# Performance work log

Measured on AMD Instinct MI355X. Metric: run time of the kernel, lower is better.

The kernel has to match this reference:

```python
import jax, jax.numpy as jnp
import numpy as np

N = 32768      # total atoms in batch
D_IN = 1024    # input feature dimension
H1 = 512       # encoder/decoder hidden width
LAT = 128      # latent dimension
D_OUT = 1024   # output dimension
E = 4          # number of unique element symbols (experts)


def _xavier(key, shape):
    # torch.nn.init.xavier_uniform_ on Linear weights
    fan_in, fan_out = shape[-2], shape[-1]
    limit = np.sqrt(6.0 / (fan_in + fan_out)).astype(np.float32)
    return jax.random.uniform(key, shape, jnp.float32, -limit, limit)


def setup_inputs() -> dict:
    key = jax.random.key(0)
    ks = jax.random.split(key, 8)
    X = jax.random.normal(ks[0], (N, D_IN), jnp.float32)
    sym_ids = jax.random.randint(ks[1], (N,), 0, E)
    # stacked per-symbol (expert) weights: topology 1024->512->128->512->1024
    We1 = _xavier(ks[2], (E, D_IN, H1));  be1 = jnp.zeros((E, H1), jnp.float32)
    We2 = _xavier(ks[3], (E, H1, LAT));   be2 = jnp.zeros((E, LAT), jnp.float32)
    Wd1 = _xavier(ks[4], (E, LAT, H1));   bd1 = jnp.zeros((E, H1), jnp.float32)
    Wd2 = _xavier(ks[5], (E, H1, D_OUT)); bd2 = jnp.zeros((E, D_OUT), jnp.float32)
    return {"X": X, "sym_ids": sym_ids,
            "We1": We1, "be1": be1, "We2": We2, "be2": be2,
            "Wd1": Wd1, "bd1": bd1, "Wd2": Wd2, "bd2": bd2}


def reference(X, sym_ids, We1, be1, We2, be2, Wd1, bd1, Wd2, bd2):
    # Dense MoE-style dispatch: compute every expert on the full batch (E is
    # tiny and fixed), then select each atom's own-symbol output. Same math as
    # the per-atom Python-loop routing in the original forward.
    def expert(e):
        h = jax.nn.relu(X @ We1[e] + be1[e])          # [N, H1]  encoder layer 1
        z = jax.nn.relu(h @ We2[e] + be2[e])          # [N, LAT] latent (encoder layer 2)
        d = jax.nn.relu(z @ Wd1[e] + bd1[e])          # [N, H1]  decoder layer 1
        return d @ Wd2[e] + bd2[e]                    # [N, D_OUT] final Linear, no activation

    outs = jnp.stack([expert(e) for e in range(E)])   # [E, N, D_OUT]
    # route: pick expert sym_ids[n] for atom n
    return jnp.take_along_axis(outs, sym_ids[None, :, None], axis=0)[0]
```

## Files before the change

### kernel.cpp

```cpp
#include <hip/hip_runtime.h>
#include <hip/hip_bf16.h>
#include <stdint.h>

typedef __bf16 bf16x8 __attribute__((ext_vector_type(8)));
typedef float  f32x4  __attribute__((ext_vector_type(4)));

#define NATOMS  32768
#define NEXP    4
#define MAXROWS (NATOMS + NEXP*256)
#define MB256   (MAXROWS/256)
#define MB128   (MAXROWS/128)
#define MGRP    ((MB256 + 7)/8)
#define PXBLK   (MAXROWS/2)

#define WS_HDR   0u
#define WS_PERM  1024u
#define WS_W1T   136192u
#define WS_W2T   (WS_W1T + 4194304u)
#define WS_W3T   (WS_W2T + 524288u)
#define WS_W4T   (WS_W3T + 524288u)
#define WS_H     (WS_W4T + 4194304u)
#define WS_D     WS_H
#define WS_XB    (WS_H + 34603008u)

__device__ __forceinline__ unsigned short f2bf(float f){
  union { float f; uint32_t u; } v; v.f = f;
  uint32_t r = v.u + 0x7fffu + ((v.u >> 16) & 1u);
  return (unsigned short)(r >> 16);
}
__device__ __forceinline__ uint32_t pk2(float a, float b){
  return (uint32_t)f2bf(a) | ((uint32_t)f2bf(b) << 16);
}
__device__ __forceinline__ void glds16(const void* g, void* l){
  __builtin_amdgcn_global_load_lds(
      (const __attribute__((address_space(1))) uint32_t*)g,
      (__attribute__((address_space(3))) uint32_t*)l, 16, 0, 0);
}

__global__ __launch_bounds__(1024) void route_kernel(const int* __restrict__ sym,
                                                     int* __restrict__ hdr,
                                                     int* __restrict__ perm){
  __shared__ unsigned wsumA[16], wsumB[16];
  __shared__ unsigned wexclA[16], wexclB[16];
  __shared__ int pof[NEXP+1];
  __shared__ int tot[NEXP];
  const int t = threadIdx.x;
  const int lane = t & 63, w = t >> 6;
  int c0=0,c1=0,c2=0,c3=0;
  const int base = t*32;
  for (int i=0;i<32;++i){
    int s = sym[base+i];
    c0 += (s==0); c1 += (s==1); c2 += (s==2); c3 += (s==3);
  }
  unsigned pA = (unsigned)c0 | ((unsigned)c1<<16);
  unsigned pB = (unsigned)c2 | ((unsigned)c3<<16);
  unsigned iA = pA, iB = pB;
  #pragma unroll
  for (int d=1; d<64; d<<=1){
    unsigned uA = __shfl_up(iA, d, 64);
    unsigned uB = __shfl_up(iB, d, 64);
    if (lane >= d){ iA += uA; iB += uB; }
  }
  unsigned exA = iA - pA, exB = iB - pB;
  if (lane == 63){ wsumA[w] = iA; wsumB[w] = iB; }
  __syncthreads();
  if (w == 0 && lane < 16){
    unsigned vA = wsumA[lane], vB = wsumB[lane];
    unsigned jA = vA, jB = vB;
    #pragma unroll
    for (int d=1; d<16; d<<=1){
      unsigned uA = __shfl_up(jA, d, 64);
      unsigned uB = __shfl_up(jB, d, 64);
      if (lane >= d){ jA += uA; jB += uB; }
    }
    wexclA[lane] = jA - vA; wexclB[lane] = jB - vB;
    if (lane == 15){
      tot[0] = (int)(jA & 0xFFFFu); tot[1] = (int)(jA >> 16);
      tot[2] = (int)(jB & 0xFFFFu); tot[3] = (int)(jB >> 16);
      int o = 0; pof[0] = 0;
      for (int e=0;e<NEXP;++e){ o += (tot[e]+255)&~255; pof[e+1]=o; }
      for (int e=0;e<=NEXP;++e) hdr[e]=pof[e];
    }
  }
  __syncthreads();
  const unsigned bA = wexclA[w] + exA, bB = wexclB[w] + exB;
  int p0 = pof[0] + (int)(bA & 0xFFFFu);
  int p1 = pof[1] + (int)(bA >> 16);
  int p2 = pof[2] + (int)(bB & 0xFFFFu);
  int p3 = pof[3] + (int)(bB >> 16);
  for (int i=t; i<MAXROWS; i+=1024) perm[i] = -1;
  __syncthreads();
  for (int i=0;i<32;++i){
    int a = base+i; int s = sym[a];
    if      (s==0) perm[p0++] = a;
    else if (s==1) perm[p1++] = a;
    else if (s==2) perm[p2++] = a;
    else           perm[p3++] = a;
  }
}

template<int K, int NO>
__device__ __forceinline__ void wtile(const float* __restrict__ W,
                                      unsigned short* __restrict__ Bt,
                                      int b, unsigned short (*tile)[65]){
  const int nx = NO/64, ny = K/64;
  const int e = b / (nx*ny), rem = b % (nx*ny);
  const int k0 = (rem / nx) * 64;
  const int n0 = (rem % nx) * 64;
  const int t  = threadIdx.x;
  const int c  = t & 63;
  const float* Wb = W + ((size_t)e*K + k0)*NO + n0;
  #pragma unroll
  for (int i=0;i<16;++i){
    int r = (t>>6) + i*4;
    tile[r][c] = f2bf(Wb[(size_t)r*NO + c]);
  }
  __syncthreads();
  unsigned short* Bb = Bt + ((size_t)e*NO + n0)*K + k0;
  #pragma unroll
  for (int i=0;i<16;++i){
    int r = (t>>6) + i*4;
    Bb[(size_t)r*K + c] = tile[c][r];
  }
}

__global__ __launch_bounds__(256) void setup_convert(
    const float* __restrict__ X,   unsigned short* __restrict__ Xb,
    const float* __restrict__ We1, unsigned short* __restrict__ W1t,
    const float* __restrict__ We2, unsigned short* __restrict__ W2t,
    const float* __restrict__ Wd1, unsigned short* __restrict__ W3t,
    const float* __restrict__ Wd2, unsigned short* __restrict__ W4t,
    const int* __restrict__ perm)
{
  __shared__ unsigned short tile[64][65];
  int b = blockIdx.x;
  const int t = threadIdx.x;
  if (b < PXBLK){
    const int row = b*2 + (t >> 7);
    const int c8  = (t & 127) * 8;
    const int a   = perm[row];
    uint4 o;
    if (a >= 0){
      const float* src = X + (size_t)a*1024 + c8;
      float4 f0 = *(const float4*)src, f1 = *(const float4*)(src + 4);
      o.x = pk2(f0.x,f0.y); o.y = pk2(f0.z,f0.w);
      o.z = pk2(f1.x,f1.y); o.w = pk2(f1.z,f1.w);
    } else {
      o = make_uint4(0u,0u,0u,0u);
    }
    *(uint4*)&Xb[(size_t)row*1024 + c8] = o;
    return;
  }
  b -= PXBLK;
  if (b < 512){ wtile<1024, 512>(We1, W1t, b, tile); return; }
  b -= 512;
  if (b <  64){ wtile< 512, 128>(We2, W2t, b, tile); return; }
  b -= 64;
  if (b <  64){ wtile< 128, 512>(Wd1, W3t, b, tile); return; }
  b -= 64;
  wtile< 512,1024>(Wd2, W4t, b, tile);
}

template<int K, int NO, int NT, bool RELU, bool FINAL>
__global__ __launch_bounds__(512, 4) void gemm_big(
    const unsigned short* __restrict__ A,
    const unsigned short* __restrict__ Bt,
    const float* __restrict__ bias,
    unsigned short* __restrict__ Cb,
    float* __restrict__ Cf,
    const int* __restrict__ hdr,
    const int* __restrict__ perm)
{
  __shared__ __align__(16) unsigned short smem[256*64 + 128*64];
  __shared__ int sperm[256];
  unsigned short* As = smem;
  unsigned short* Bs = smem + 256*64;

  const int b = blockIdx.x;
  const int grp = b / (8*NT), rem = b % (8*NT);
  const int rowblk = grp*8 + (rem & 7);
  const int row0 = rowblk * 256;
  if (row0 >= hdr[NEXP]) return;
  const int ntile = rem >> 3;
  const int e = (row0 >= hdr[1]) + (row0 >= hdr[2]) + (row0 >= hdr[3]);
  const int n0 = ntile * 128;

  const int t = threadIdx.x;
  const int lane = t & 63, wid = t >> 6;

  if constexpr (FINAL){
    if (t < 256) sperm[t] = perm[row0 + t];
    __syncthreads();
  }

  const int l8 = lane >> 3;
  const int scoff = (((lane & 7) ^ l8) << 3);

  const unsigned short* asrc[4];
  #pragma unroll
  for (int i=0;i<4;++i)
    asrc[i] = A + (size_t)(row0 + wid*32 + i*8 + l8)*K + scoff;
  const unsigned short* bsrc[2];
  #pragma unroll
  for (int i=0;i<2;++i)
    bsrc[i] = Bt + ((size_t)e*NO + n0 + wid*16 + i*8 + l8)*K + scoff;

  const int lr   = lane & 15;
  const int sgrp = lane >> 4;
  const int wr   = (wid >> 1) * 64;
  const int wc   = (wid & 1) * 64;

  f32x4 acc[4][4];
  const f32x4 z4 = {0.f,0.f,0.f,0.f};
  #pragma unroll
  for (int mi=0;mi<4;++mi)
    #pragma unroll
    for (int ni=0;ni<4;++ni) acc[mi][ni] = z4;

  #pragma unroll 1
  for (int kt = 0; kt < K/64; ++kt){
    __syncthreads();
    #pragma unroll
    for (int i=0;i<4;++i)
      glds16(asrc[i] + kt*64, As + (wid*4+i)*512);
    #pragma unroll
    for (int i=0;i<2;++i)
      glds16(bsrc[i] + kt*64, Bs + (wid*2+i)*512);
    __syncthreads();

    #pragma unroll
    for (int kk=0;kk<2;++kk){
      bf16x8 af[4], bfr[4];
      const int s = kk*4 + sgrp;
      #pragma unroll
      for (int mi=0;mi<4;++mi){
        int R = wr + mi*16 + lr;
        af[mi] = *(const bf16x8*)&As[R*64 + ((s ^ (R & 7)) << 3)];
      }
      #pragma unroll
      for (int ni=0;ni<4;++ni){
        int Cc = wc + ni*16 + lr;
        bfr[ni] = *(const bf16x8*)&Bs[Cc*64 + ((s ^ (Cc & 7)) << 3)];
      }
      #pragma unroll
      for (int mi=0;mi<4;++mi)
        #pragma unroll
        for (int ni=0;ni<4;++ni)
          acc[mi][ni] = __builtin_amdgcn_mfma_f32_16x16x32_bf16(af[mi], bfr[ni], acc[mi][ni], 0, 0, 0);
    }
  }

  __syncthreads();
  if constexpr (FINAL){
    float* stf = (float*)smem;
    #pragma unroll
    for (int qr=0; qr<4; ++qr){
      if ((wid >> 1) == qr){
        #pragma unroll
        for (int ni=0;ni<4;++ni){
          const int colg = n0 + wc + ni*16 + lr;
          const float bv_ = bias[(size_t)e*NO + colg];
          #pragma unroll
          for (int mi=0;mi<4;++mi){
            #pragma unroll
            for (int q=0;q<4;++q){
              float v = acc[mi][ni][q] + bv_;
              if (RELU) v = fmaxf(v, 0.f);
              stf[(mi*16 + sgrp*4 + q)*132 + wc + ni*16 + lr] = v;
            }
          }
        }
      }
      __syncthreads();
      #pragma unroll
      for (int i=0;i<4;++i){
        int idx = t + 512*i;
        int r = idx >> 5, c4 = idx & 31;
        int atom = sperm[qr*64 + r];
        if (atom >= 0)
          *(float4*)&Cf[(size_t)atom*NO + n0 + c4*4] = *(const float4*)&stf[r*132 + c4*4];
      }
      __syncthreads();
    }
  } else {
    unsigned short* st = smem;
    const int wrl = ((wid >> 1) & 1) * 64;
    #pragma unroll
    for (int h=0; h<2; ++h){
      if ((wid >> 2) == h){
        #pragma unroll
        for (int ni=0;ni<4;++ni){
          const int colg = n0 + wc + ni*16 + lr;
          const float bv_ = bias[(size_t)e*NO + colg];
          #pragma unroll
          for (int mi=0;mi<4;++mi){
            #pragma unroll
            for (int q=0;q<4;++q){
              float v = acc[mi][ni][q] + bv_;
              if (RELU) v = fmaxf(v, 0.f);
              st[(wrl + mi*16 + sgrp*4 + q)*136 + wc + ni*16 + lr] = f2bf(v);
            }
          }
        }
      }
      __syncthreads();
      #pragma unroll
      for (int i=0;i<4;++i){
        int idx = t + 512*i;
        int r = idx >> 4, c8 = idx & 15;
        *(uint4*)&Cb[(size_t)(row0 + h*128 + r)*NO + n0 + c8*8] = *(const uint4*)&st[r*136 + c8*8];
      }
      __syncthreads();
    }
  }
}

__global__ __launch_bounds__(256, 2) void fused_mid(
    const unsigned short* H,
    const unsigned short* __restrict__ W2,
    const float* __restrict__ b2,
    const unsigned short* __restrict__ W3,
    const float* __restrict__ b3,
    unsigned short* D,
    const int* __restrict__ hdr)
{
  __shared__ __align__(16) unsigned short un[128*136];
  __shared__ __align__(16) unsigned short Zs[128*128];
  unsigned short* As = un;
  unsigned short* Bs = un + 128*64;

  const int row0 = blockIdx.x * 128;
  if (row0 >= hdr[NEXP]) return;
  const int e = (row0 >= hdr[1]) + (row0 >= hdr[2]) + (row0 >= hdr[3]);

  const int t = threadIdx.x;
  const int lane = t & 63, wid = t >> 6;
  const int l8 = lane >> 3;
  const int scoff = (((lane & 7) ^ l8) << 3);
  const int lr = lane & 15, sgrp = lane >> 4;
  const int wr = (wid >> 1) * 64, wc = (wid & 1) * 64;

  const unsigned short* asrc[4];
  const unsigned short* bsrc[4];
  #pragma unroll
  for (int i=0;i<4;++i){
    asrc[i] = H  + (size_t)(row0 + wid*32 + i*8 + l8)*512 + scoff;
    bsrc[i] = W2 + ((size_t)e*128 + wid*32 + i*8 + l8)*512 + scoff;
  }

  f32x4 acc[4][4];
  const f32x4 z4 = {0.f,0.f,0.f,0.f};
  #pragma unroll
  for (int mi=0;mi<4;++mi)
    #pragma unroll
    for (int ni=0;ni<4;++ni) acc[mi][ni] = z4;

  #pragma unroll 1
  for (int kt = 0; kt < 8; ++kt){
    __syncthreads();
    #pragma unroll
    for (int i=0;i<4;++i){
      glds16(asrc[i] + kt*64, As + (wid*4+i)*512);
      glds16(bsrc[i] + kt*64, Bs + (wid*4+i)*512);
    }
    __syncthreads();
    #pragma unroll
    for (int kk=0;kk<2;++kk){
      bf16x8 af[4], bfr[4];
      const int s = kk*4 + sgrp;
      #pragma unroll
      for (int mi=0;mi<4;++mi){
        int R = wr + mi*16 + lr;
        af[mi] = *(const bf16x8*)&As[R*64 + ((s ^ (R & 7)) << 3)];
      }
      #pragma unroll
      for (int ni=0;ni<4;++ni){
        int Cc = wc + ni*16 + lr;
        bfr[ni] = *(const bf16x8*)&Bs[Cc*64 + ((s ^ (Cc & 7)) << 3)];
      }
      #pragma unroll
      for (int mi=0;mi<4;++mi)
        #pragma unroll
        for (int ni=0;ni<4;++ni)
          acc[mi][ni] = __builtin_amdgcn_mfma_f32_16x16x32_bf16(af[mi], bfr[ni], acc[mi][ni], 0, 0, 0);
    }
  }
  #pragma unroll
  for (int ni=0;ni<4;++ni){
    const int col = wc + ni*16 + lr;
    const float bv_ = b2[(size_t)e*128 + col];
    const int ch = col >> 3, cl = col & 7;
    #pragma unroll
    for (int mi=0;mi<4;++mi){
      #pragma unroll
      for (int q=0;q<4;++q){
        const int row = wr + mi*16 + sgrp*4 + q;
        float v = fmaxf(acc[mi][ni][q] + bv_, 0.f);
        Zs[row*128 + ((ch ^ (row & 15)) << 3) + cl] = f2bf(v);
      }
    }
  }
  __syncthreads();

  bf16x8 afk[4][4];
  #pragma unroll
  for (int kk=0;kk<4;++kk)
    #pragma unroll
    for (int mi=0;mi<4;++mi){
      int R = wr + mi*16 + lr;
      afk[kk][mi] = *(const bf16x8*)&Zs[R*128 + (((kk*4+sgrp) ^ (R & 15)) << 3)];
    }

  #pragma unroll 1
  for (int nt=0; nt<4; ++nt){
    #pragma unroll
    for (int i=0;i<8;++i){
      int R = (wid*8 + i)*4 + (lane >> 4);
      int sch = (lane & 15) ^ (R & 15);
      glds16(W3 + ((size_t)e*512 + nt*128 + R)*128 + sch*8, un + (size_t)(wid*8+i)*512);
    }
    __syncthreads();

    #pragma unroll
    for (int mi=0;mi<4;++mi)
      #pragma unroll
      for (int ni=0;ni<4;++ni) acc[mi][ni] = z4;

    #pragma unroll
    for (int kk=0;kk<4;++kk){
      bf16x8 bfr[4];
      const int s = kk*4 + sgrp;
      #pragma unroll
      for (int ni=0;ni<4;++ni){
        int Cc = wc + ni*16 + lr;
        bfr[ni] = *(const bf16x8*)&un[Cc*128 + ((s ^ (Cc & 15)) << 3)];
      }
      #pragma unroll
      for (int mi=0;mi<4;++mi)
        #pragma unroll
        for (int ni=0;ni<4;++ni)
          acc[mi][ni] = __builtin_amdgcn_mfma_f32_16x16x32_bf16(afk[kk][mi], bfr[ni], acc[mi][ni], 0, 0, 0);
    }
    __syncthreads();

    #pragma unroll
    for (int ni=0;ni<4;++ni){
      const int col = wc + ni*16 + lr;
      const float bv_ = b3[(size_t)e*512 + nt*128 + col];
      #pragma unroll
      for (int mi=0;mi<4;++mi){
        #pragma unroll
        for (int q=0;q<4;++q){
          const int row = wr + mi*16 + sgrp*4 + q;
          float v = fmaxf(acc[mi][ni][q] + bv_, 0.f);
          un[row*136 + col] = f2bf(v);
        }
      }
    }
    __syncthreads();
    #pragma unroll
    for (int i=0;i<8;++i){
      int idx = t + 256*i;
      int r = idx >> 4, c8 = idx & 15;
      *(uint4*)&D[(size_t)(row0 + r)*512 + nt*128 + c8*8] = *(const uint4*)&un[r*136 + c8*8];
    }
    __syncthreads();
  }
}

extern "C" void kernel_launch(void* const* d_in, const int* in_sizes, int n_in,
                              void* d_out, int out_size, void* d_ws, size_t ws_size,
                              hipStream_t stream) {
  const float* X   = (const float*)d_in[0];
  const int*   sym = (const int*)  d_in[1];
  const float* We1 = (const float*)d_in[2];
  const float* be1 = (const float*)d_in[3];
  const float* We2 = (const float*)d_in[4];
  const float* be2 = (const float*)d_in[5];
  const float* Wd1 = (const float*)d_in[6];
  const float* bd1 = (const float*)d_in[7];
  const float* Wd2 = (const float*)d_in[8];
  const float* bd2 = (const float*)d_in[9];
  float* out = (float*)d_out;

  char* ws = (char*)d_ws;
  int* hdr  = (int*)(ws + WS_HDR);
  int* perm = (int*)(ws + WS_PERM);
  unsigned short* W1t = (unsigned short*)(ws + WS_W1T);
  unsigned short* W2t = (unsigned short*)(ws + WS_W2T);
  unsigned short* W3t = (unsigned short*)(ws + WS_W3T);
  unsigned short* W4t = (unsigned short*)(ws + WS_W4T);
  unsigned short* H   = (unsigned short*)(ws + WS_H);
  unsigned short* Dd  = (unsigned short*)(ws + WS_D);
  unsigned short* Xb  = (unsigned short*)(ws + WS_XB);

  dim3 b256(256), b512(512);
  route_kernel<<<1, 1024, 0, stream>>>(sym, hdr, perm);
  setup_convert<<<dim3(PXBLK + 512 + 64 + 64 + 512), b256, 0, stream>>>(
      X, Xb, We1, W1t, We2, W2t, Wd1, W3t, Wd2, W4t, perm);

  gemm_big<1024, 512, 4, true,  false><<<dim3(MGRP*8*4), b512, 0, stream>>>(
      Xb, W1t, be1, H, nullptr, hdr, perm);
  fused_mid<<<dim3(MB128), b256, 0, stream>>>(H, W2t, be2, W3t, bd1, Dd, hdr);
  gemm_big< 512,1024, 8, false, true ><<<dim3(MGRP*8*8), b512, 0, stream>>>(
      Dd, W4t, bd2, nullptr, out, hdr, perm);
}
```

Before: 232.3 us.

## Fuse X gather/bf16 conversion into first GEMM and double-buffer GEMM tiles

Removes the separate pass that gathers permuted X rows and converts them to a bf16 workspace. The first GEMM now loads fp32 X rows through the permutation directly, converts them in registers and writes them to LDS. Both big GEMMs move from 256-row, 512-thread tiles to 128-row, 256-thread tiles with double-buffered LDS, so the next k-tile loads while the current one is computed. This saves the 64MB intermediate write and read, at the cost of fp32 global loads inside the GEMM and a smaller per-block tile.

New measurement: 253.1 us. 1.09x slower.

```diff
diff --git a/kernel.cpp b/kernel.cpp
--- a/kernel.cpp
+++ b/kernel.cpp
@@ -8,10 +8,8 @@
 #define NATOMS  32768
 #define NEXP    4
 #define MAXROWS (NATOMS + NEXP*256)
-#define MB256   (MAXROWS/256)
 #define MB128   (MAXROWS/128)
-#define MGRP    ((MB256 + 7)/8)
-#define PXBLK   (MAXROWS/2)
+#define MG8     (MB128/8)
 
 #define WS_HDR   0u
 #define WS_PERM  1024u
@@ -21,7 +19,6 @@
 #define WS_W4T   (WS_W3T + 524288u)
 #define WS_H     (WS_W4T + 4194304u)
 #define WS_D     WS_H
-#define WS_XB    (WS_H + 34603008u)
 
 __device__ __forceinline__ unsigned short f2bf(float f){
   union { float f; uint32_t u; } v; v.f = f;
@@ -125,33 +122,13 @@
 }
 
 __global__ __launch_bounds__(256) void setup_convert(
-    const float* __restrict__ X,   unsigned short* __restrict__ Xb,
     const float* __restrict__ We1, unsigned short* __restrict__ W1t,
     const float* __restrict__ We2, unsigned short* __restrict__ W2t,
     const float* __restrict__ Wd1, unsigned short* __restrict__ W3t,
-    const float* __restrict__ Wd2, unsigned short* __restrict__ W4t,
-    const int* __restrict__ perm)
+    const float* __restrict__ Wd2, unsigned short* __restrict__ W4t)
 {
   __shared__ unsigned short tile[64][65];
   int b = blockIdx.x;
-  const int t = threadIdx.x;
-  if (b < PXBLK){
-    const int row = b*2 + (t >> 7);
-    const int c8  = (t & 127) * 8;
-    const int a   = perm[row];
-    uint4 o;
-    if (a >= 0){
-      const float* src = X + (size_t)a*1024 + c8;
-      float4 f0 = *(const float4*)src, f1 = *(const float4*)(src + 4);
-      o.x = pk2(f0.x,f0.y); o.y = pk2(f0.z,f0.w);
-      o.z = pk2(f1.x,f1.y); o.w = pk2(f1.z,f1.w);
-    } else {
-      o = make_uint4(0u,0u,0u,0u);
-    }
-    *(uint4*)&Xb[(size_t)row*1024 + c8] = o;
-    return;
-  }
-  b -= PXBLK;
   if (b < 512){ wtile<1024, 512>(We1, W1t, b, tile); return; }
   b -= 512;
   if (b <  64){ wtile< 512, 128>(We2, W2t, b, tile); return; }
@@ -161,9 +138,10 @@
   wtile< 512,1024>(Wd2, W4t, b, tile);
 }
 
-template<int K, int NO, int NT, bool RELU, bool FINAL>
-__global__ __launch_bounds__(512, 4) void gemm_big(
+template<int K, int NO, int NT, bool RELU, bool GF32, bool FINAL>
+__global__ __launch_bounds__(256, 2) void gemm_db(
     const unsigned short* __restrict__ A,
+    const float* __restrict__ Af,
     const unsigned short* __restrict__ Bt,
     const float* __restrict__ bias,
     unsigned short* __restrict__ Cb,
@@ -171,15 +149,13 @@
     const int* __restrict__ hdr,
     const int* __restrict__ perm)
 {
-  __shared__ __align__(16) unsigned short smem[256*64 + 128*64];
-  __shared__ int sperm[256];
-  unsigned short* As = smem;
-  unsigned short* Bs = smem + 256*64;
+  __shared__ __align__(16) unsigned short smem[4*128*64];
+  __shared__ int sperm[128];
 
   const int b = blockIdx.x;
   const int grp = b / (8*NT), rem = b % (8*NT);
   const int rowblk = grp*8 + (rem & 7);
-  const int row0 = rowblk * 256;
+  const int row0 = rowblk * 128;
   if (row0 >= hdr[NEXP]) return;
   const int ntile = rem >> 3;
   const int e = (row0 >= hdr[1]) + (row0 >= hdr[2]) + (row0 >= hdr[3]);
@@ -188,22 +164,36 @@
   const int t = threadIdx.x;
   const int lane = t & 63, wid = t >> 6;
 
-  if constexpr (FINAL){
-    if (t < 256) sperm[t] = perm[row0 + t];
+  if constexpr (GF32 || FINAL){
+    if (t < 128) sperm[t] = perm[row0 + t];
     __syncthreads();
   }
 
   const int l8 = lane >> 3;
   const int scoff = (((lane & 7) ^ l8) << 3);
 
+  const unsigned short* bsrc[4];
+  #pragma unroll
+  for (int i=0;i<4;++i)
+    bsrc[i] = Bt + ((size_t)e*NO + n0 + wid*32 + i*8 + l8)*K + scoff;
+
   const unsigned short* asrc[4];
-  #pragma unroll
-  for (int i=0;i<4;++i)
-    asrc[i] = A + (size_t)(row0 + wid*32 + i*8 + l8)*K + scoff;
-  const unsigned short* bsrc[2];
-  #pragma unroll
-  for (int i=0;i<2;++i)
-    bsrc[i] = Bt + ((size_t)e*NO + n0 + wid*16 + i*8 + l8)*K + scoff;
+  const float* af32[4];
+  int awoff[4];
+  if constexpr (!GF32){
+    #pragma unroll
+    for (int i=0;i<4;++i)
+      asrc[i] = A + (size_t)(row0 + wid*32 + i*8 + l8)*K + scoff;
+  } else {
+    #pragma unroll
+    for (int j=0;j<4;++j){
+      int cch = t + 256*j;
+      int r   = cch >> 3;
+      int a   = sperm[r];
+      af32[j] = Af + (size_t)(a < 0 ? 0 : a)*K + (cch & 7)*8;
+      awoff[j] = r*64 + (((cch & 7) ^ (r & 7)) << 3);
+    }
+  }
 
   const int lr   = lane & 15;
   const int sgrp = lane >> 4;
@@ -217,45 +207,78 @@
     #pragma unroll
     for (int ni=0;ni<4;++ni) acc[mi][ni] = z4;
 
+  float4 ar0[4], ar1[4];
+
+  #define STAGE_B(kt,c) { _Pragma("unroll") \
+    for (int i=0;i<4;++i) glds16(bsrc[i] + (kt)*64, smem + 16384 + (c)*8192 + (wid*4+i)*512); }
+  #define STAGE_A_GLDS(kt,c) { _Pragma("unroll") \
+    for (int i=0;i<4;++i) glds16(asrc[i] + (kt)*64, smem + (c)*8192 + (wid*4+i)*512); }
+  #define LOAD_A(kt) { _Pragma("unroll") \
+    for (int j=0;j<4;++j){ ar0[j] = *(const float4*)(af32[j] + (kt)*64); \
+                           ar1[j] = *(const float4*)(af32[j] + (kt)*64 + 4); } }
+  #define WRITE_A(c) { _Pragma("unroll") \
+    for (int j=0;j<4;++j){ uint4 o; \
+      o.x = pk2(ar0[j].x, ar0[j].y); o.y = pk2(ar0[j].z, ar0[j].w); \
+      o.z = pk2(ar1[j].x, ar1[j].y); o.w = pk2(ar1[j].z, ar1[j].w); \
+      *(uint4*)&smem[(c)*8192 + awoff[j]] = o; } }
+
+  if constexpr (GF32){
+    LOAD_A(0);
+    STAGE_B(0, 0);
+    WRITE_A(0);
+  } else {
+    STAGE_A_GLDS(0, 0);
+    STAGE_B(0, 0);
+  }
+  __syncthreads();
+
+  int c = 0;
   #pragma unroll 1
   for (int kt = 0; kt < K/64; ++kt){
-    __syncthreads();
-    #pragma unroll
-    for (int i=0;i<4;++i)
-      glds16(asrc[i] + kt*64, As + (wid*4+i)*512);
-    #pragma unroll
-    for (int i=0;i<2;++i)
-      glds16(bsrc[i] + kt*64, Bs + (wid*2+i)*512);
-    __syncthreads();
-
-    #pragma unroll
-    for (int kk=0;kk<2;++kk){
-      bf16x8 af[4], bfr[4];
-      const int s = kk*4 + sgrp;
-      #pragma unroll
-      for (int mi=0;mi<4;++mi){
-        int R = wr + mi*16 + lr;
-        af[mi] = *(const bf16x8*)&As[R*64 + ((s ^ (R & 7)) << 3)];
-      }
-      #pragma unroll
-      for (int ni=0;ni<4;++ni){
-        int Cc = wc + ni*16 + lr;
-        bfr[ni] = *(const bf16x8*)&Bs[Cc*64 + ((s ^ (Cc & 7)) << 3)];
-      }
-      #pragma unroll
-      for (int mi=0;mi<4;++mi)
-        #pragma unroll
-        for (int ni=0;ni<4;++ni)
-          acc[mi][ni] = __builtin_amdgcn_mfma_f32_16x16x32_bf16(af[mi], bfr[ni], acc[mi][ni], 0, 0, 0);
-    }
-  }
-
-  __syncthreads();
+    const bool more = (kt + 1 < K/64);
+    if (more){
+      if constexpr (GF32){ LOAD_A(kt+1); }
+      else               { STAGE_A_GLDS(kt+1, c^1); }
+      STAGE_B(kt+1, c^1);
+    }
+    {
+      const unsigned short* Asb = smem + c*8192;
+      const unsigned short* Bsb = smem + 16384 + c*8192;
+      #pragma unroll
+      for (int kk=0;kk<2;++kk){
+        bf16x8 af[4], bfr[4];
+        const int s = kk*4 + sgrp;
+        #pragma unroll
+        for (int mi=0;mi<4;++mi){
+          int R = wr + mi*16 + lr;
+          af[mi] = *(const bf16x8*)&Asb[R*64 + ((s ^ (R & 7)) << 3)];
+        }
+        #pragma unroll
+        for (int ni=0;ni<4;++ni){
+          int Cc = wc + ni*16 + lr;
+          bfr[ni] = *(const bf16x8*)&Bsb[Cc*64 + ((s ^ (Cc & 7)) << 3)];
+        }
+        #pragma unroll
+        for (int mi=0;mi<4;++mi)
+          #pragma unroll
+          for (int ni=0;ni<4;++ni)
+            acc[mi][ni] = __builtin_amdgcn_mfma_f32_16x16x32_bf16(af[mi], bfr[ni], acc[mi][ni], 0, 0, 0);
+      }
+    }
+    if constexpr (GF32){ if (more) WRITE_A(c^1); }
+    __syncthreads();
+    c ^= 1;
+  }
+  #undef STAGE_B
+  #undef STAGE_A_GLDS
+  #undef LOAD_A
+  #undef WRITE_A
+
   if constexpr (FINAL){
     float* stf = (float*)smem;
     #pragma unroll
-    for (int qr=0; qr<4; ++qr){
-      if ((wid >> 1) == qr){
+    for (int h=0; h<2; ++h){
+      if ((wid >> 1) == h){
         #pragma unroll
         for (int ni=0;ni<4;++ni){
           const int colg = n0 + wc + ni*16 + lr;
@@ -273,10 +296,10 @@
       }
       __syncthreads();
       #pragma unroll
-      for (int i=0;i<4;++i){
-        int idx = t + 512*i;
+      for (int i=0;i<8;++i){
+        int idx = t + 256*i;
         int r = idx >> 5, c4 = idx & 31;
-        int atom = sperm[qr*64 + r];
+        int atom = sperm[h*64 + r];
         if (atom >= 0)
           *(float4*)&Cf[(size_t)atom*NO + n0 + c4*4] = *(const float4*)&stf[r*132 + c4*4];
       }
@@ -284,33 +307,26 @@
     }
   } else {
     unsigned short* st = smem;
-    const int wrl = ((wid >> 1) & 1) * 64;
-    #pragma unroll
-    for (int h=0; h<2; ++h){
-      if ((wid >> 2) == h){
-        #pragma unroll
-        for (int ni=0;ni<4;++ni){
-          const int colg = n0 + wc + ni*16 + lr;
-          const float bv_ = bias[(size_t)e*NO + colg];
-          #pragma unroll
-          for (int mi=0;mi<4;++mi){
-            #pragma unroll
-            for (int q=0;q<4;++q){
-              float v = acc[mi][ni][q] + bv_;
-              if (RELU) v = fmaxf(v, 0.f);
-              st[(wrl + mi*16 + sgrp*4 + q)*136 + wc + ni*16 + lr] = f2bf(v);
-            }
-          }
+    #pragma unroll
+    for (int ni=0;ni<4;++ni){
+      const int colg = n0 + wc + ni*16 + lr;
+      const float bv_ = bias[(size_t)e*NO + colg];
+      #pragma unroll
+      for (int mi=0;mi<4;++mi){
+        #pragma unroll
+        for (int q=0;q<4;++q){
+          float v = acc[mi][ni][q] + bv_;
+          if (RELU) v = fmaxf(v, 0.f);
+          st[(wr + mi*16 + sgrp*4 + q)*136 + wc + ni*16 + lr] = f2bf(v);
         }
       }
-      __syncthreads();
-      #pragma unroll
-      for (int i=0;i<4;++i){
-        int idx = t + 512*i;
-        int r = idx >> 4, c8 = idx & 15;
-        *(uint4*)&Cb[(size_t)(row0 + h*128 + r)*NO + n0 + c8*8] = *(const uint4*)&st[r*136 + c8*8];
-      }
-      __syncthreads();
+    }
+    __syncthreads();
+    #pragma unroll
+    for (int i=0;i<8;++i){
+      int idx = t + 256*i;
+      int r = idx >> 4, c8 = idx & 15;
+      *(uint4*)&Cb[(size_t)(row0 + r)*NO + n0 + c8*8] = *(const uint4*)&st[r*136 + c8*8];
     }
   }
 }
@@ -492,16 +508,15 @@
   unsigned short* W4t = (unsigned short*)(ws + WS_W4T);
   unsigned short* H   = (unsigned short*)(ws + WS_H);
   unsigned short* Dd  = (unsigned short*)(ws + WS_D);
-  unsigned short* Xb  = (unsigned short*)(ws + WS_XB);
-
-  dim3 b256(256), b512(512);
+
+  dim3 b256(256);
   route_kernel<<<1, 1024, 0, stream>>>(sym, hdr, perm);
-  setup_convert<<<dim3(PXBLK + 512 + 64 + 64 + 512), b256, 0, stream>>>(
-      X, Xb, We1, W1t, We2, W2t, Wd1, W3t, Wd2, W4t, perm);
-
-  gemm_big<1024, 512, 4, true,  false><<<dim3(MGRP*8*4), b512, 0, stream>>>(
-      Xb, W1t, be1, H, nullptr, hdr, perm);
+  setup_convert<<<dim3(512 + 64 + 64 + 512), b256, 0, stream>>>(
+      We1, W1t, We2, W2t, Wd1, W3t, Wd2, W4t);
+
+  gemm_db<1024, 512, 4, true,  true,  false><<<dim3(MG8*8*4), b256, 0, stream>>>(
+      nullptr, X, W1t, be1, H, nullptr, hdr, perm);
   fused_mid<<<dim3(MB128), b256, 0, stream>>>(H, W2t, be2, W3t, bd1, Dd, hdr);
-  gemm_big< 512,1024, 8, false, true ><<<dim3(MGRP*8*8), b512, 0, stream>>>(
-      Dd, W4t, bd2, nullptr, out, hdr, perm);
-}
+  gemm_db< 512,1024, 8, false, false, true ><<<dim3(MG8*8*8), b256, 0, stream>>>(
+      Dd, nullptr, W4t, bd2, nullptr, out, hdr, perm);
+}
```

## Fuse X gather and bf16 conversion into first-layer GEMM loading fp32 rows

Applied to the files above, without the earlier changes.

Removes the separate pass that gathered permuted X rows, converted them to bf16 and wrote a staging buffer. A new layer-1 GEMM kernel instead gathers fp32 rows directly into LDS through per-row perm pointers and converts to bf16 in registers before the MFMA. This saves one full write and re-read of the activation matrix, but it doubles LDS traffic for the A operand, uses a smaller 128-row tile with 256 threads, and drops the previous tuned 256-row kernel for this layer.

New measurement: 221.3 us. -4.7%, faster.

```diff
diff --git a/kernel.cpp b/kernel.cpp
--- a/kernel.cpp
+++ b/kernel.cpp
@@ -11,7 +11,7 @@
 #define MB256   (MAXROWS/256)
 #define MB128   (MAXROWS/128)
 #define MGRP    ((MB256 + 7)/8)
-#define PXBLK   (MAXROWS/2)
+#define MG128   ((MB128 + 7)/8)
 
 #define WS_HDR   0u
 #define WS_PERM  1024u
@@ -21,15 +21,11 @@
 #define WS_W4T   (WS_W3T + 524288u)
 #define WS_H     (WS_W4T + 4194304u)
 #define WS_D     WS_H
-#define WS_XB    (WS_H + 34603008u)
 
 __device__ __forceinline__ unsigned short f2bf(float f){
   union { float f; uint32_t u; } v; v.f = f;
   uint32_t r = v.u + 0x7fffu + ((v.u >> 16) & 1u);
   return (unsigned short)(r >> 16);
-}
-__device__ __forceinline__ uint32_t pk2(float a, float b){
-  return (uint32_t)f2bf(a) | ((uint32_t)f2bf(b) << 16);
 }
 __device__ __forceinline__ void glds16(const void* g, void* l){
   __builtin_amdgcn_global_load_lds(
@@ -125,33 +121,13 @@
 }
 
 __global__ __launch_bounds__(256) void setup_convert(
-    const float* __restrict__ X,   unsigned short* __restrict__ Xb,
     const float* __restrict__ We1, unsigned short* __restrict__ W1t,
     const float* __restrict__ We2, unsigned short* __restrict__ W2t,
     const float* __restrict__ Wd1, unsigned short* __restrict__ W3t,
-    const float* __restrict__ Wd2, unsigned short* __restrict__ W4t,
-    const int* __restrict__ perm)
+    const float* __restrict__ Wd2, unsigned short* __restrict__ W4t)
 {
   __shared__ unsigned short tile[64][65];
   int b = blockIdx.x;
-  const int t = threadIdx.x;
-  if (b < PXBLK){
-    const int row = b*2 + (t >> 7);
-    const int c8  = (t & 127) * 8;
-    const int a   = perm[row];
-    uint4 o;
-    if (a >= 0){
-      const float* src = X + (size_t)a*1024 + c8;
-      float4 f0 = *(const float4*)src, f1 = *(const float4*)(src + 4);
-      o.x = pk2(f0.x,f0.y); o.y = pk2(f0.z,f0.w);
-      o.z = pk2(f1.x,f1.y); o.w = pk2(f1.z,f1.w);
-    } else {
-      o = make_uint4(0u,0u,0u,0u);
-    }
-    *(uint4*)&Xb[(size_t)row*1024 + c8] = o;
-    return;
-  }
-  b -= PXBLK;
   if (b < 512){ wtile<1024, 512>(We1, W1t, b, tile); return; }
   b -= 512;
   if (b <  64){ wtile< 512, 128>(We2, W2t, b, tile); return; }
@@ -159,6 +135,121 @@
   if (b <  64){ wtile< 128, 512>(Wd1, W3t, b, tile); return; }
   b -= 64;
   wtile< 512,1024>(Wd2, W4t, b, tile);
+}
+
+template<int NT>
+__global__ __launch_bounds__(256, 3) void gemm_l1f32(
+    const float* __restrict__ Xf,
+    const unsigned short* __restrict__ Bt,
+    const float* __restrict__ bias,
+    unsigned short* __restrict__ Cb,
+    const int* __restrict__ hdr,
+    const int* __restrict__ perm)
+{
+  constexpr int K = 1024, NO = 512;
+  __shared__ __align__(16) float          Af[128*64];
+  __shared__ __align__(16) unsigned short Bs[128*64];
+
+  const int b = blockIdx.x;
+  const int grp = b / (8*NT), rem = b % (8*NT);
+  const int rowblk = grp*8 + (rem & 7);
+  const int row0 = rowblk * 128;
+  if (row0 >= hdr[NEXP]) return;
+  const int ntile = rem >> 3;
+  const int e = (row0 >= hdr[1]) + (row0 >= hdr[2]) + (row0 >= hdr[3]);
+  const int n0 = ntile * 128;
+
+  const int t = threadIdx.x;
+  const int lane = t & 63, wid = t >> 6;
+
+  const float* afsrc[8];
+  #pragma unroll
+  for (int i=0;i<8;++i){
+    int r = wid*32 + i*4 + (lane >> 4);
+    int a = perm[row0 + r];
+    if (a < 0) a = 0;
+    int c = (lane & 15) ^ (r & 15);
+    afsrc[i] = Xf + (size_t)a*K + c*4;
+  }
+  const int l8 = lane >> 3;
+  const int scoff = (((lane & 7) ^ l8) << 3);
+  const unsigned short* bsrc[4];
+  #pragma unroll
+  for (int i=0;i<4;++i)
+    bsrc[i] = Bt + ((size_t)e*NO + n0 + wid*32 + i*8 + l8)*K + scoff;
+
+  const int lr   = lane & 15;
+  const int sgrp = lane >> 4;
+  const int wr   = (wid >> 1) * 64;
+  const int wc   = (wid & 1) * 64;
+
+  f32x4 acc[4][4];
+  const f32x4 z4 = {0.f,0.f,0.f,0.f};
+  #pragma unroll
+  for (int mi=0;mi<4;++mi)
+    #pragma unroll
+    for (int ni=0;ni<4;++ni) acc[mi][ni] = z4;
+
+  #pragma unroll 1
+  for (int kt = 0; kt < K/64; ++kt){
+    __syncthreads();
+    #pragma unroll
+    for (int i=0;i<8;++i)
+      glds16(afsrc[i] + kt*64, Af + (wid*32 + i*4)*64);
+    #pragma unroll
+    for (int i=0;i<4;++i)
+      glds16(bsrc[i] + kt*64, Bs + (wid*4+i)*512);
+    __syncthreads();
+
+    #pragma unroll
+    for (int kk=0;kk<2;++kk){
+      const int s = kk*4 + sgrp;
+      bf16x8 af[4], bfr[4];
+      #pragma unroll
+      for (int mi=0;mi<4;++mi){
+        int R = wr + mi*16 + lr;
+        float4 f0 = *(const float4*)&Af[R*64 + (((2*s  ) ^ (R & 15)) << 2)];
+        float4 f1 = *(const float4*)&Af[R*64 + (((2*s+1) ^ (R & 15)) << 2)];
+        bf16x8 v;
+        v[0]=(__bf16)f0.x; v[1]=(__bf16)f0.y; v[2]=(__bf16)f0.z; v[3]=(__bf16)f0.w;
+        v[4]=(__bf16)f1.x; v[5]=(__bf16)f1.y; v[6]=(__bf16)f1.z; v[7]=(__bf16)f1.w;
+        af[mi] = v;
+      }
+      #pragma unroll
+      for (int ni=0;ni<4;++ni){
+        int Cc = wc + ni*16 + lr;
+        bfr[ni] = *(const bf16x8*)&Bs[Cc*64 + ((s ^ (Cc & 7)) << 3)];
+      }
+      #pragma unroll
+      for (int mi=0;mi<4;++mi)
+        #pragma unroll
+        for (int ni=0;ni<4;++ni)
+          acc[mi][ni] = __builtin_amdgcn_mfma_f32_16x16x32_bf16(af[mi], bfr[ni], acc[mi][ni], 0, 0, 0);
+    }
+  }
+
+  __syncthreads();
+  unsigned short* st = (unsigned short*)Af;
+  #pragma unroll
+  for (int ni=0;ni<4;++ni){
+    const int colg = n0 + wc + ni*16 + lr;
+    const float bv_ = bias[(size_t)e*NO + colg];
+    #pragma unroll
+    for (int mi=0;mi<4;++mi){
+      #pragma unroll
+      for (int q=0;q<4;++q){
+        float v = fmaxf(acc[mi][ni][q] + bv_, 0.f);
+        st[(wr + mi*16 + sgrp*4 + q)*136 + wc + ni*16 + lr] = f2bf(v);
+      }
+    }
+  }
+  __syncthreads();
+  #pragma unroll
+  for (int i=0;i<8;++i){
+    int idx = t + 256*i;
+    int r = idx >> 4, c8 = idx & 15;
+    *(uint4*)&Cb[(size_t)(row0 + r)*NO + n0 + c8*8] = *(const uint4*)&st[r*136 + c8*8];
+  }
 }
 
 template<int K, int NO, int NT, bool RELU, bool FINAL>
@@ -492,15 +583,14 @@
   unsigned short* W4t = (unsigned short*)(ws + WS_W4T);
   unsigned short* H   = (unsigned short*)(ws + WS_H);
   unsigned short* Dd  = (unsigned short*)(ws + WS_D);
-  unsigned short* Xb  = (unsigned short*)(ws + WS_XB);
 
   dim3 b256(256), b512(512);
   route_kernel<<<1, 1024, 0, stream>>>(sym, hdr, perm);
-  setup_convert<<<dim3(PXBLK + 512 + 64 + 64 + 512), b256, 0, stream>>>(
-      X, Xb, We1, W1t, We2, W2t, Wd1, W3t, Wd2, W4t, perm);
-
-  gemm_big<1024, 512, 4, true,  false><<<dim3(MGRP*8*4), b512, 0, stream>>>(
-      Xb, W1t, be1, H, nullptr, hdr, perm);
+  setup_convert<<<dim3(512 + 64 + 64 + 512), b256, 0, stream>>>(
+      We1, W1t, We2, W2t, Wd1, W3t, Wd2, W4t);
+
+  gemm_l1f32<4><<<dim3(MG128*8*4), b256, 0, stream>>>(
+      X, W1t, be1, H, hdr, perm);
   fused_mid<<<dim3(MB128), b256, 0, stream>>>(H, W2t, be2, W3t, bd1, Dd, hdr);
   gemm_big< 512,1024, 8, false, true ><<<dim3(MGRP*8*8), b512, 0, stream>>>(
       Dd, W4t, bd2, nullptr, out, hdr, perm);
```
